# Optimization experiments

Hardware: AMD Instinct MI355X
Metric: run time of the kernel (lower is better)

Reference implementation:

```python
import jax, jax.numpy as jnp
import numpy as np

D_MODEL = 1024
BATCH = 4
SEQ = 4096


def setup_inputs() -> dict:
    key = jax.random.key(0)
    kx, kwz, kwh = jax.random.split(key, 3)
    scale = 1.0 / np.sqrt(D_MODEL)
    x = jax.random.normal(kx, (BATCH, SEQ, D_MODEL), dtype=jnp.float32)
    Wz = jax.random.normal(kwz, (D_MODEL, D_MODEL), dtype=jnp.float32) * scale
    bz = jnp.zeros((D_MODEL,), dtype=jnp.float32)
    Wh = jax.random.normal(kwh, (D_MODEL, D_MODEL), dtype=jnp.float32) * scale
    bh = jnp.zeros((D_MODEL,), dtype=jnp.float32)
    return {"x": x, "Wz": Wz, "bz": bz, "Wh": Wh, "bh": bh}


def _parallel_scan_real(a, b):
    # h_t = a_t * h_{t-1} + b_t via log-depth associative scan along time axis.
    def binary_op(left, right):
        a_l, b_l = left
        a_r, b_r = right
        return (a_l * a_r, a_r * b_l + b_r)
    _, h = jax.lax.associative_scan(binary_op, (a, b), axis=1)
    return h


def reference(x, Wz, bz, Wh, bh):
    # x: [B, T, D]
    z = jax.nn.sigmoid(jnp.einsum('btd,de->bte', x, Wz) + bz)  # update gate
    h_tilde = jnp.einsum('btd,de->bte', x, Wh) + bh            # candidate
    return _parallel_scan_real(1.0 - z, z * h_tilde)           # [B, T, D]
```

## Files before the change

### kernel.cpp

```cpp
#include <hip/hip_runtime.h>
#include <hip/hip_bf16.h>
#include <stdint.h>

#define D_MODEL 1024
#define BATCH   4
#define SEQ     4096
#define M_TOTAL (BATCH*SEQ)
#define KDIM    D_MODEL
#define NTOT    2048

#define NC 128
#define CL (SEQ/NC)

#define BM 256
#define BN 256
#define BK 32
#define NT (KDIM/BK)

typedef __bf16 bf16x8 __attribute__((ext_vector_type(8)));
typedef float  f32x4  __attribute__((ext_vector_type(4)));
typedef unsigned short u16x4 __attribute__((ext_vector_type(4)));

static __device__ __forceinline__ unsigned short f2bf(float f) {
  unsigned u = __builtin_bit_cast(unsigned, f);
  u += 0x7FFFu + ((u >> 16) & 1u);
  return (unsigned short)(u >> 16);
}
static __device__ __forceinline__ float bf2f(unsigned short u) {
  return __builtin_bit_cast(float, (unsigned)u << 16);
}

__global__ __launch_bounds__(256) void k_cvt_x(const float* __restrict__ x,
                                               unsigned short* __restrict__ xb) {
  int i = blockIdx.x * 256 + threadIdx.x;
  float4 v = ((const float4*)x)[i];
  ushort4 o;
  o.x = f2bf(v.x); o.y = f2bf(v.y); o.z = f2bf(v.z); o.w = f2bf(v.w);
  ((ushort4*)xb)[i] = o;
}

__global__ void k_cvt_wT(const float* __restrict__ Wz, const float* __restrict__ Wh,
                         unsigned short* __restrict__ WzT, unsigned short* __restrict__ WhT) {
  __shared__ float tile[32][33];
  const float* W = blockIdx.z ? Wh : Wz;
  unsigned short* O = blockIdx.z ? WhT : WzT;
  int bx = blockIdx.x * 32;
  int by = blockIdx.y * 32;
  int tx = threadIdx.x, ty = threadIdx.y;
  for (int yy = ty; yy < 32; yy += 8)
    tile[yy][tx] = W[(size_t)(by + yy) * D_MODEL + bx + tx];
  __syncthreads();
  for (int yy = ty; yy < 32; yy += 8)
    O[(size_t)(bx + yy) * D_MODEL + by + tx] = f2bf(tile[tx][yy]);
}

__global__ __launch_bounds__(512, 2) void k_gemm8(
    const unsigned short* __restrict__ xb,
    const unsigned short* __restrict__ Wall,
    unsigned short* __restrict__ P, unsigned short* __restrict__ Q)
{
  __shared__ __attribute__((aligned(16))) unsigned short lds[3 * 16384];

  const int tid  = threadIdx.x;
  const int wave = tid >> 6;
  const int lane = tid & 63;
  const int m0 = blockIdx.x * BM;
  const int n0 = blockIdx.y * BN;
  const int wr = wave >> 2;
  const int wc = wave & 3;
  const int lr = lane & 15;
  const int lc = lane >> 4;

  const int p0 = wave * 2, p1 = wave * 2 + 1;
  const int c0 = p0 >> 2, rb0 = p0 & 3;
  const int c1 = p1 >> 2, rb1 = p1 & 3;

  f32x4 acc[8][4];
  #pragma unroll
  for (int i = 0; i < 8; ++i)
    #pragma unroll
    for (int j = 0; j < 4; ++j) acc[i][j] = (f32x4){0.f, 0.f, 0.f, 0.f};

  auto stage = [&](int kt, int bufb) {
    const int kb = kt * BK;
    unsigned short* ldsA = &lds[bufb * 16384];
    unsigned short* ldsB = ldsA + 8192;
    const unsigned short* a0 = xb   + (size_t)(m0 + rb0*64 + lane) * KDIM + kb + c0*8;
    const unsigned short* a1 = xb   + (size_t)(m0 + rb1*64 + lane) * KDIM + kb + c1*8;
    const unsigned short* b0 = Wall + (size_t)(n0 + rb0*64 + lane) * KDIM + kb + c0*8;
    const unsigned short* b1 = Wall + (size_t)(n0 + rb1*64 + lane) * KDIM + kb + c1*8;
    __builtin_amdgcn_global_load_lds((const __attribute__((address_space(1))) unsigned int*)a0,
        (__attribute__((address_space(3))) unsigned int*)(ldsA + (c0*256 + rb0*64)*8), 16, 0, 0);
    __builtin_amdgcn_global_load_lds((const __attribute__((address_space(1))) unsigned int*)a1,
        (__attribute__((address_space(3))) unsigned int*)(ldsA + (c1*256 + rb1*64)*8), 16, 0, 0);
    __builtin_amdgcn_global_load_lds((const __attribute__((address_space(1))) unsigned int*)b0,
        (__attribute__((address_space(3))) unsigned int*)(ldsB + (c0*256 + rb0*64)*8), 16, 0, 0);
    __builtin_amdgcn_global_load_lds((const __attribute__((address_space(1))) unsigned int*)b1,
        (__attribute__((address_space(3))) unsigned int*)(ldsB + (c1*256 + rb1*64)*8), 16, 0, 0);
  };

  stage(0, 0);
  stage(1, 1);
  asm volatile("s_waitcnt vmcnt(4)" ::: "memory");
  __builtin_amdgcn_s_barrier();

  const int aoff = (lc * 256 + wr * 128 + lr) * 8;
  const int boff = (lc * 256 + wc * 64  + lr) * 8;

  int buf = 0;
  for (int kt = 0; kt < NT; ++kt) {
    if (kt + 2 < NT) {
      int db = buf + 2; if (db >= 3) db -= 3;
      stage(kt + 2, db);
    }

    const unsigned short* bufA = &lds[buf * 16384];
    const unsigned short* bufB = bufA + 8192;

    bf16x8 bfrag[4];
    #pragma unroll
    for (int nf = 0; nf < 4; ++nf)
      bfrag[nf] = *(const bf16x8*)(bufB + boff + nf * 128);
    bf16x8 afrag[4];
    #pragma unroll
    for (int mf = 0; mf < 4; ++mf)
      afrag[mf] = *(const bf16x8*)(bufA + aoff + mf * 128);

    __builtin_amdgcn_s_setprio(1);
    #pragma unroll
    for (int mf = 0; mf < 4; ++mf)
      #pragma unroll
      for (int nf = 0; nf < 4; ++nf)
        acc[mf][nf] = __builtin_amdgcn_mfma_f32_16x16x32_bf16(afrag[mf], bfrag[nf], acc[mf][nf], 0, 0, 0);
    __builtin_amdgcn_s_setprio(0);

    #pragma unroll
    for (int mf = 0; mf < 4; ++mf)
      afrag[mf] = *(const bf16x8*)(bufA + aoff + (mf + 4) * 128);

    __builtin_amdgcn_s_setprio(1);
    #pragma unroll
    for (int mf = 0; mf < 4; ++mf)
      #pragma unroll
      for (int nf = 0; nf < 4; ++nf)
        acc[mf + 4][nf] = __builtin_amdgcn_mfma_f32_16x16x32_bf16(afrag[mf], bfrag[nf], acc[mf + 4][nf], 0, 0, 0);
    __builtin_amdgcn_s_setprio(0);

    if (kt < NT - 2) asm volatile("s_waitcnt vmcnt(4)" ::: "memory");
    else             asm volatile("s_waitcnt vmcnt(0)" ::: "memory");
    __builtin_amdgcn_s_barrier();
    buf = (buf == 2) ? 0 : buf + 1;
  }

  unsigned short* Cout = (n0 < 1024) ? P : Q;
  const int colb = (n0 < 1024) ? n0 : (n0 - 1024);
  const int cb = lane & 15;
  const int rb4 = (lane >> 4) * 4;
  #pragma unroll
  for (int mf = 0; mf < 8; ++mf) {
    #pragma unroll
    for (int nf = 0; nf < 4; ++nf) {
      const size_t col  = (size_t)(colb + wc * 64 + nf * 16 + cb);
      const size_t row0 = (size_t)(m0 + wr * 128 + mf * 16 + rb4);
      #pragma unroll
      for (int r = 0; r < 4; ++r)
        Cout[(row0 + r) * D_MODEL + col] = f2bf(acc[mf][nf][r]);
    }
  }
}

__global__ __launch_bounds__(256) void k_scan_agg(
    const unsigned short* __restrict__ P, const unsigned short* __restrict__ Q,
    const float* __restrict__ bz, const float* __restrict__ bh,
    float* __restrict__ Aagg, float* __restrict__ Bagg)
{
  int c = blockIdx.x & (NC - 1);
  int b = blockIdx.x >> 7;
  int d = threadIdx.x * 4;
  f32x4 vbz = *(const f32x4*)(bz + d);
  f32x4 vbh = *(const f32x4*)(bh + d);
  f32x4 A = {1.f, 1.f, 1.f, 1.f}, Bv = {0.f, 0.f, 0.f, 0.f};
  size_t base = ((size_t)b * SEQ + (size_t)c * CL) * D_MODEL + d;
  for (int t = 0; t < CL; ++t) {
    u16x4 pu = *(const u16x4*)(P + base + (size_t)t * D_MODEL);
    u16x4 qu = *(const u16x4*)(Q + base + (size_t)t * D_MODEL);
    #pragma unroll
    for (int r = 0; r < 4; ++r) {
      float z = 1.f / (1.f + __expf(-(bf2f(pu[r]) + vbz[r])));
      float a = 1.f - z;
      float bb = z * (bf2f(qu[r]) + vbh[r]);
      Bv[r] = a * Bv[r] + bb;
      A[r]  = a * A[r];
    }
  }
  size_t o = ((size_t)b * NC + c) * D_MODEL + d;
  *(f32x4*)(Aagg + o) = A;
  *(f32x4*)(Bagg + o) = Bv;
}

__global__ __launch_bounds__(256) void k_scan_chunks(
    const float* __restrict__ Aagg, const float* __restrict__ Bagg,
    float* __restrict__ Pref)
{
  int idx = blockIdx.x * 256 + threadIdx.x;
  int b = idx >> 10, d = idx & 1023;
  float h = 0.f;
  for (int cc = 0; cc < NC; ++cc) {
    size_t o = ((size_t)b * NC + cc) * D_MODEL + d;
    Pref[o] = h;
    h = Aagg[o] * h + Bagg[o];
  }
}

__global__ __launch_bounds__(256) void k_scan_apply(
    const unsigned short* __restrict__ P, const unsigned short* __restrict__ Q,
    const float* __restrict__ bz, const float* __restrict__ bh,
    const float* __restrict__ Pref, float* __restrict__ out)
{
  int c = blockIdx.x & (NC - 1);
  int b = blockIdx.x >> 7;
  int d = threadIdx.x * 4;
  f32x4 vbz = *(const f32x4*)(bz + d);
  f32x4 vbh = *(const f32x4*)(bh + d);
  f32x4 h = *(const f32x4*)(Pref + ((size_t)b * NC + c) * D_MODEL + d);
  size_t base = ((size_t)b * SEQ + (size_t)c * CL) * D_MODEL + d;
  for (int t = 0; t < CL; ++t) {
    u16x4 pu = *(const u16x4*)(P + base + (size_t)t * D_MODEL);
    u16x4 qu = *(const u16x4*)(Q + base + (size_t)t * D_MODEL);
    #pragma unroll
    for (int r = 0; r < 4; ++r) {
      float z = 1.f / (1.f + __expf(-(bf2f(pu[r]) + vbz[r])));
      float a = 1.f - z;
      h[r] = a * h[r] + z * (bf2f(qu[r]) + vbh[r]);
    }
    *(f32x4*)(out + base + (size_t)t * D_MODEL) = h;
  }
}

extern "C" void kernel_launch(void* const* d_in, const int* in_sizes, int n_in,
                              void* d_out, int out_size, void* d_ws, size_t ws_size,
                              hipStream_t stream)
{
  const float* x  = (const float*)d_in[0];
  const float* Wz = (const float*)d_in[1];
  const float* bz = (const float*)d_in[2];
  const float* Wh = (const float*)d_in[3];
  const float* bh = (const float*)d_in[4];

  char* ws = (char*)d_ws;
  unsigned short* xb   = (unsigned short*)(ws);
  unsigned short* Wall = (unsigned short*)(ws + 33554432);
  unsigned short* Pb   = (unsigned short*)(ws + 37748736);
  unsigned short* Qb   = (unsigned short*)(ws + 71303168);
  float* Aagg = (float*)(ws + 104857600);
  float* Bagg = (float*)(ws + 106954752);
  float* Pref = (float*)(ws + 109051904);
  float* out  = (float*)d_out;

  k_cvt_x<<<M_TOTAL * D_MODEL / 4 / 256, 256, 0, stream>>>(x, xb);
  k_cvt_wT<<<dim3(32, 32, 2), dim3(32, 8), 0, stream>>>(Wz, Wh, Wall, Wall + (size_t)1024 * 1024);
  k_gemm8<<<dim3(M_TOTAL / BM, NTOT / BN), 512, 0, stream>>>(xb, Wall, Pb, Qb);
  k_scan_agg<<<BATCH * NC, 256, 0, stream>>>(Pb, Qb, bz, bh, Aagg, Bagg);
  k_scan_chunks<<<BATCH * D_MODEL / 256, 256, 0, stream>>>(Aagg, Bagg, Pref);
  k_scan_apply<<<BATCH * NC, 256, 0, stream>>>(Pb, Qb, bz, bh, Pref, out);
}
```

Measured before the change: 162.4 us.

## Fuse chunked scan into one kernel with flag-based inter-block prefix

Merges the three scan kernels (chunk aggregate, sequential chunk prefix, apply) into a single kernel. Each block publishes its chunk aggregates with a release flag, then waits on the flags of all earlier chunks and recomputes its own prefix by walking back over them. This removes two kernel launches and the serial per-channel prefix pass. In exchange it adds a flag-zeroing launch and O(c) prefix work per block, and it relies on all 512 blocks being co-resident or scheduled in order to avoid spin deadlock.

```diff
diff --git a/kernel.cpp b/kernel.cpp
--- a/kernel.cpp
+++ b/kernel.cpp
@@ -6,11 +6,11 @@
 #define BATCH   4
 #define SEQ     4096
 #define M_TOTAL (BATCH*SEQ)
-#define KDIM    D_MODEL
+#define KDIM    1024
 #define NTOT    2048
 
-#define NC 128
-#define CL (SEQ/NC)
+#define NCH 128
+#define CL (SEQ/NCH)
 
 #define BM 256
 #define BN 256
@@ -69,7 +69,6 @@
   const int wr = wave >> 2;
   const int wc = wave & 3;
   const int lr = lane & 15;
-  const int lc = lane >> 4;
 
   const int p0 = wave * 2, p1 = wave * 2 + 1;
   const int c0 = p0 >> 2, rb0 = p0 & 3;
@@ -104,6 +103,7 @@
   asm volatile("s_waitcnt vmcnt(4)" ::: "memory");
   __builtin_amdgcn_s_barrier();
 
+  const int lc  = lane >> 4;
   const int aoff = (lc * 256 + wr * 128 + lr) * 8;
   const int boff = (lc * 256 + wc * 64  + lr) * 8;
 
@@ -169,18 +169,25 @@
   }
 }
 
-__global__ __launch_bounds__(256) void k_scan_agg(
+__global__ __launch_bounds__(256) void k_zero_flags(int* __restrict__ flags) {
+  flags[threadIdx.x] = 0;
+  flags[threadIdx.x + 256] = 0;
+}
+
+__global__ __launch_bounds__(256) void k_scan_fused(
     const unsigned short* __restrict__ P, const unsigned short* __restrict__ Q,
     const float* __restrict__ bz, const float* __restrict__ bh,
-    float* __restrict__ Aagg, float* __restrict__ Bagg)
+    float* __restrict__ Aagg, float* __restrict__ Bagg,
+    int* __restrict__ flags, float* __restrict__ out)
 {
-  int c = blockIdx.x & (NC - 1);
-  int b = blockIdx.x >> 7;
-  int d = threadIdx.x * 4;
-  f32x4 vbz = *(const f32x4*)(bz + d);
-  f32x4 vbh = *(const f32x4*)(bh + d);
+  const int c = blockIdx.x & (NCH - 1);
+  const int b = blockIdx.x >> 7;
+  const int d = threadIdx.x * 4;
+  const f32x4 vbz = *(const f32x4*)(bz + d);
+  const f32x4 vbh = *(const f32x4*)(bh + d);
+  const size_t base = ((size_t)b * SEQ + (size_t)c * CL) * D_MODEL + d;
+
   f32x4 A = {1.f, 1.f, 1.f, 1.f}, Bv = {0.f, 0.f, 0.f, 0.f};
-  size_t base = ((size_t)b * SEQ + (size_t)c * CL) * D_MODEL + d;
   for (int t = 0; t < CL; ++t) {
     u16x4 pu = *(const u16x4*)(P + base + (size_t)t * D_MODEL);
     u16x4 qu = *(const u16x4*)(Q + base + (size_t)t * D_MODEL);
@@ -188,42 +195,36 @@
     for (int r = 0; r < 4; ++r) {
       float z = 1.f / (1.f + __expf(-(bf2f(pu[r]) + vbz[r])));
       float a = 1.f - z;
-      float bb = z * (bf2f(qu[r]) + vbh[r]);
-      Bv[r] = a * Bv[r] + bb;
+      Bv[r] = a * Bv[r] + z * (bf2f(qu[r]) + vbh[r]);
       A[r]  = a * A[r];
     }
   }
-  size_t o = ((size_t)b * NC + c) * D_MODEL + d;
+  const size_t o = ((size_t)b * NCH + c) * D_MODEL + d;
   *(f32x4*)(Aagg + o) = A;
   *(f32x4*)(Bagg + o) = Bv;
-}
-
-__global__ __launch_bounds__(256) void k_scan_chunks(
-    const float* __restrict__ Aagg, const float* __restrict__ Bagg,
-    float* __restrict__ Pref)
-{
-  int idx = blockIdx.x * 256 + threadIdx.x;
-  int b = idx >> 10, d = idx & 1023;
-  float h = 0.f;
-  for (int cc = 0; cc < NC; ++cc) {
-    size_t o = ((size_t)b * NC + cc) * D_MODEL + d;
-    Pref[o] = h;
-    h = Aagg[o] * h + Bagg[o];
-  }
-}
-
-__global__ __launch_bounds__(256) void k_scan_apply(
-    const unsigned short* __restrict__ P, const unsigned short* __restrict__ Q,
-    const float* __restrict__ bz, const float* __restrict__ bh,
-    const float* __restrict__ Pref, float* __restrict__ out)
-{
-  int c = blockIdx.x & (NC - 1);
-  int b = blockIdx.x >> 7;
-  int d = threadIdx.x * 4;
-  f32x4 vbz = *(const f32x4*)(bz + d);
-  f32x4 vbh = *(const f32x4*)(bh + d);
-  f32x4 h = *(const f32x4*)(Pref + ((size_t)b * NC + c) * D_MODEL + d);
-  size_t base = ((size_t)b * SEQ + (size_t)c * CL) * D_MODEL + d;
+  __threadfence();
+  __syncthreads();
+  if (threadIdx.x == 0)
+    __hip_atomic_store(&flags[b * NCH + c], 1, __ATOMIC_RELEASE, __HIP_MEMORY_SCOPE_AGENT);
+
+  f32x4 h = {0.f, 0.f, 0.f, 0.f};
+  if (c > 0) {
+    if ((int)threadIdx.x < c) {
+      while (__hip_atomic_load(&flags[b * NCH + threadIdx.x],
+                               __ATOMIC_ACQUIRE, __HIP_MEMORY_SCOPE_AGENT) == 0) {}
+    }
+    __syncthreads();
+    f32x4 Ar = {1.f, 1.f, 1.f, 1.f};
+    #pragma unroll 2
+    for (int j = c - 1; j >= 0; --j) {
+      const size_t oj = ((size_t)b * NCH + j) * D_MODEL + d;
+      f32x4 Aj = *(const f32x4*)(Aagg + oj);
+      f32x4 Bj = *(const f32x4*)(Bagg + oj);
+      h  = Ar * Bj + h;
+      Ar = Ar * Aj;
+    }
+  }
+
   for (int t = 0; t < CL; ++t) {
     u16x4 pu = *(const u16x4*)(P + base + (size_t)t * D_MODEL);
     u16x4 qu = *(const u16x4*)(Q + base + (size_t)t * D_MODEL);
@@ -254,13 +255,12 @@
   unsigned short* Qb   = (unsigned short*)(ws + 71303168);
   float* Aagg = (float*)(ws + 104857600);
   float* Bagg = (float*)(ws + 106954752);
-  float* Pref = (float*)(ws + 109051904);
+  int*   flags = (int*)(ws + 109051904);
   float* out  = (float*)d_out;
 
   k_cvt_x<<<M_TOTAL * D_MODEL / 4 / 256, 256, 0, stream>>>(x, xb);
   k_cvt_wT<<<dim3(32, 32, 2), dim3(32, 8), 0, stream>>>(Wz, Wh, Wall, Wall + (size_t)1024 * 1024);
+  k_zero_flags<<<1, 256, 0, stream>>>(flags);
   k_gemm8<<<dim3(M_TOTAL / BM, NTOT / BN), 512, 0, stream>>>(xb, Wall, Pb, Qb);
-  k_scan_agg<<<BATCH * NC, 256, 0, stream>>>(Pb, Qb, bz, bh, Aagg, Bagg);
-  k_scan_chunks<<<BATCH * D_MODEL / 256, 256, 0, stream>>>(Aagg, Bagg, Pref);
-  k_scan_apply<<<BATCH * NC, 256, 0, stream>>>(Pb, Qb, bz, bh, Pref, out);
-}
+  k_scan_fused<<<BATCH * NCH, 256, 0, stream>>>(Pb, Qb, bz, bh, Aagg, Bagg, flags, out);
+}
```

Result: slower. 242.7 us (+49.4%).
